# Optimization experiments

Hardware: AMD Instinct MI355X
Metric: run time of the kernel (lower is better)

The kernel has to match this reference:

```python
import jax, jax.numpy as jnp
import numpy as np
from jax import lax

KH, KW = 3, 3  # hardcoded in the original extract_patches sizes=(1,3,3,1)


def setup_inputs() -> dict:
    key = jax.random.key(0)
    k1, k2, k3 = jax.random.split(key, 3)
    B, H, W, C = 32, 56, 56, 128
    num_och = 256
    x = jax.random.normal(k1, (B, H, W, C), dtype=jnp.float32)
    w = jax.random.normal(k2, (num_och, KH * KW * C), dtype=jnp.float32) * 0.05
    b = jax.random.normal(k3, (num_och,), dtype=jnp.float32) * 0.05
    return {"x": x, "w": w, "b": b}


def reference(x, w, b):
    # Original: extract_patches (SAME, stride 1, 3x3) -> tile num_och times ->
    # elementwise multiply with w -> reduce_sum over patch axis -> + bias.
    # This is exactly a 3x3 SAME conv: patch layout is (ky, kx, cin) row-major,
    # matching tf.image.extract_patches depth ordering.
    num_och = w.shape[0]
    cin = x.shape[-1]
    # (num_och, KH*KW*C) -> (KH, KW, C, num_och) for HWIO kernel layout
    kernel = w.reshape(num_och, KH, KW, cin).transpose(1, 2, 3, 0)
    out = lax.conv_general_dilated(
        x, kernel,
        window_strides=(1, 1),
        padding="SAME",
        dimension_numbers=("NHWC", "HWIO", "NHWC"),
    )
    return out + b
```

## Files before the change

### kernel.cpp

```cpp
#include <hip/hip_runtime.h>
#include <hip/hip_bf16.h>

#define HH   56
#define WW_  56
#define CIN  128
#define OCH  256
#define NPIX (32*56*56)
#define NX   (NPIX*CIN)
#define NW   (OCH*9*CIN)
#define XB_BYTES ((size_t)NX*2)
#define WB_BYTES ((size_t)NW*2)
#define ZP_OFF   (XB_BYTES + WB_BYTES)
#define WS_NEEDED (ZP_OFF + 256)

#define NT   18
#define SLOT 65536
#define THREADS 512

typedef __attribute__((ext_vector_type(8))) short bf16x8;
typedef __attribute__((ext_vector_type(4))) float f32x4;
typedef __attribute__((address_space(1))) void v_g;
typedef __attribute__((address_space(3))) void v_l;

__device__ __forceinline__ unsigned short f2bf(float f) {
  union { float f; unsigned u; } v; v.f = f;
  unsigned r = v.u + 0x7FFF + ((v.u >> 16) & 1);
  return (unsigned short)(r >> 16);
}

__global__ __launch_bounds__(256) void convert_kern(
    const float* __restrict__ x, const float* __restrict__ w,
    char* __restrict__ ws)
{
  if (blockIdx.x == 0 && threadIdx.x < 64)
    ((float*)(ws + ZP_OFF))[threadIdx.x] = 0.f;

  unsigned short* out = (unsigned short*)ws;
  const int NT8 = (NX + NW) / 8;
  for (int i = blockIdx.x * blockDim.x + threadIdx.x; i < NT8;
       i += gridDim.x * blockDim.x) {
    const int e = i * 8;
    const float* src = (e < NX) ? (x + e) : (w + (e - NX));
    const float4 a = ((const float4*)src)[0];
    const float4 b = ((const float4*)src)[1];
    union { bf16x8 v; unsigned short u[8]; } p;
    p.u[0] = f2bf(a.x); p.u[1] = f2bf(a.y); p.u[2] = f2bf(a.z); p.u[3] = f2bf(a.w);
    p.u[4] = f2bf(b.x); p.u[5] = f2bf(b.y); p.u[6] = f2bf(b.z); p.u[7] = f2bf(b.w);
    *(bf16x8*)(out + e) = p.v;
  }
}

__global__ __launch_bounds__(THREADS, 2) void conv_gemm6(
    const char* __restrict__ ws, const float* __restrict__ bias,
    float* __restrict__ out)
{
  __shared__ char lds[2 * SLOT];

  const char* xb = ws;
  const char* wb = ws + XB_BYTES;
  const char* zp = ws + ZP_OFF;

  const int tid  = threadIdx.x;
  const int lane = tid & 63;

  const int bid = blockIdx.x;
  const int m0  = ((bid & 7) * 49 + (bid >> 3)) * 256;

  const int r0  = tid >> 3;
  const int chk = ((tid & 7) ^ (r0 & 7)) * 16;
  const char* zpc = zp + chk;

  int pixA[4], phA[4], pwA[4];
  const char* bsrc[4];
#pragma unroll
  for (int l = 0; l < 4; ++l) {
    const int r  = r0 + l * 64;
    const int p  = m0 + r;
    const int pb = p / 3136;
    const int phw = p - pb * 3136;
    phA[l] = phw / 56;
    pwA[l] = phw - phA[l] * 56;
    pixA[l] = p;
    bsrc[l] = wb + (size_t)r * 2304 + chk;
  }

  const int fr = lane & 15;
  const int fq = lane >> 4;
  const int wv = tid >> 6;
  const int wr = wv >> 2;
  const int wc = wv & 3;

  int aoffs[8], boffs[4];
#pragma unroll
  for (int mi = 0; mi < 8; ++mi) {
    const int r = wr * 128 + mi * 16 + fr;
    aoffs[mi] = r * 128 + ((fq * 16) ^ ((r & 7) << 4));
  }
#pragma unroll
  for (int nj = 0; nj < 4; ++nj) {
    const int c = wc * 64 + nj * 16 + fr;
    boffs[nj] = 32768 + c * 128 + ((fq * 16) ^ ((c & 7) << 4));
  }

  f32x4 acc[8][4];
  const f32x4 zero4 = {0.f, 0.f, 0.f, 0.f};
#pragma unroll
  for (int mi = 0; mi < 8; ++mi)
#pragma unroll
    for (int nj = 0; nj < 4; ++nj) acc[mi][nj] = zero4;

#define STAGE(tt, dst) do {                                                   \
    const int kpos_ = (tt) >> 1, kh_ = (tt) & 1;                              \
    const int ky_ = kpos_ / 3;                                                \
    const int dy_ = ky_ - 1, dx_ = kpos_ - ky_ * 3 - 1;                       \
    _Pragma("unroll")                                                         \
    for (int l = 0; l < 4; ++l) {                                             \
      const int ih_ = phA[l] + dy_, iw_ = pwA[l] + dx_;                       \
      const bool v_ = ((unsigned)ih_ < 56u) & ((unsigned)iw_ < 56u);          \
      const char* ga_ = v_ ? (xb + (size_t)(pixA[l] + dy_ * 56 + dx_) * 256   \
                                 + kh_ * 128 + chk)                           \
                           : zpc;                                             \
      __builtin_amdgcn_global_load_lds((const v_g*)ga_,                       \
          (v_l*)((dst) + l * 8192 + tid * 16), 16, 0, 0);                     \
    }                                                                         \
    _Pragma("unroll")                                                         \
    for (int l = 0; l < 4; ++l)                                               \
      __builtin_amdgcn_global_load_lds((const v_g*)(bsrc[l] + (tt) * 128),    \
          (v_l*)((dst) + 32768 + l * 8192 + tid * 16), 16, 0, 0);             \
  } while (0)

#define PHASE(src, ks, mq, LOADB) do {                                        \
    bf16x8 Aq[4];                                                             \
    _Pragma("unroll")                                                         \
    for (int i = 0; i < 4; ++i)                                               \
      Aq[i] = *(const bf16x8*)((src) + (aoffs[(mq) * 4 + i] ^ ((ks) << 6)));  \
    if (LOADB) {                                                              \
      _Pragma("unroll")                                                       \
      for (int j = 0; j < 4; ++j)                                             \
        Bq[j] = *(const bf16x8*)((src) + (boffs[j] ^ ((ks) << 6)));           \
    }                                                                         \
    __builtin_amdgcn_sched_barrier(0);                                        \
    __builtin_amdgcn_s_barrier();                                             \
    __builtin_amdgcn_sched_barrier(0);                                        \
    __builtin_amdgcn_s_setprio(1);                                            \
    _Pragma("unroll")                                                         \
    for (int i = 0; i < 4; ++i)                                               \
      _Pragma("unroll")                                                       \
      for (int j = 0; j < 4; ++j)                                             \
        acc[(mq) * 4 + i][j] = __builtin_amdgcn_mfma_f32_16x16x32_bf16(       \
            Aq[i], Bq[j], acc[(mq) * 4 + i][j], 0, 0, 0);                     \
    __builtin_amdgcn_s_setprio(0);                                            \
    __builtin_amdgcn_sched_barrier(0);                                        \
    __builtin_amdgcn_s_barrier();                                             \
  } while (0)

#define COMPUTE(src) do {                                                     \
    bf16x8 Bq[4];                                                             \
    PHASE(src, 0, 0, true);                                                   \
    PHASE(src, 0, 1, false);                                                  \
    PHASE(src, 1, 0, true);                                                   \
    PHASE(src, 1, 1, false);                                                  \
  } while (0)

  char* s0 = lds;
  char* s1 = lds + SLOT;

  STAGE(0, s0);

#pragma unroll
  for (int t = 0; t < NT - 1; ++t) {
    STAGE(t + 1, ((t + 1) & 1) ? s1 : s0);
    asm volatile("s_waitcnt vmcnt(8)" ::: "memory");
    __builtin_amdgcn_s_barrier();
    __builtin_amdgcn_sched_barrier(0);
    COMPUTE((t & 1) ? s1 : s0);
  }

  asm volatile("s_waitcnt vmcnt(0)" ::: "memory");
  __builtin_amdgcn_s_barrier();
  __builtin_amdgcn_sched_barrier(0);
  COMPUTE(((NT - 1) & 1) ? s1 : s0);

#undef STAGE
#undef PHASE
#undef COMPUTE

  float bv[4];
#pragma unroll
  for (int nj = 0; nj < 4; ++nj) bv[nj] = bias[wc * 64 + nj * 16 + fr];

#pragma unroll
  for (int mi = 0; mi < 8; ++mi) {
#pragma unroll
    for (int j = 0; j < 4; ++j) {
      const int prow = m0 + wr * 128 + mi * 16 + fq * 4 + j;
      float* orow = out + (size_t)prow * OCH + wc * 64 + fr;
#pragma unroll
      for (int nj = 0; nj < 4; ++nj)
        orow[nj * 16] = acc[mi][nj][j] + bv[nj];
    }
  }
}

__global__ __launch_bounds__(256) void conv3x3_mfma_fb(
    const float* __restrict__ x, const float* __restrict__ w,
    const float* __restrict__ bias, float* __restrict__ out)
{
  __shared__ alignas(16) unsigned char As[128 * 64];
  __shared__ alignas(16) unsigned char Bs[128 * 64];

  const int tid = threadIdx.x;
  const int m0 = (blockIdx.x >> 1) * 128;
  const int n0 = (blockIdx.x & 1) * 128;

  const int srow = tid >> 1;
  const int soff = (tid & 1) * 16;

  const int p   = m0 + srow;
  const int pb  = p / (HH * WW_);
  const int phw = p - pb * (HH * WW_);
  const int ph  = phw / WW_;
  const int pw  = phw - ph * WW_;

  const float* xrow = x + ((size_t)((pb * HH + ph) * WW_ + pw)) * CIN + soff;
  const float* wrow = w + (size_t)(n0 + srow) * (9 * CIN) + soff;

  const int sw0 = (srow * 64 + soff * 2)      ^ ((srow & 7) << 4);
  const int sw1 = (srow * 64 + soff * 2 + 16) ^ ((srow & 7) << 4);

  const int lane = tid & 63;
  const int wv = tid >> 6;
  const int wm = (wv >> 1) * 64;
  const int wn = (wv & 1) * 64;
  const int fr = lane & 15;
  const int fq = lane >> 4;

  int aoff[4], boff[4];
#pragma unroll
  for (int i = 0; i < 4; ++i) {
    const int r = wm + i * 16 + fr;
    aoff[i] = (r * 64 + fq * 16) ^ ((r & 7) << 4);
    const int c = wn + i * 16 + fr;
    boff[i] = (c * 64 + fq * 16) ^ ((c & 7) << 4);
  }

  f32x4 acc[4][4];
  const f32x4 zero4 = {0.f, 0.f, 0.f, 0.f};
#pragma unroll
  for (int i = 0; i < 4; ++i)
#pragma unroll
    for (int j = 0; j < 4; ++j) acc[i][j] = zero4;

#pragma unroll 1
  for (int kpos = 0; kpos < 9; ++kpos) {
    const int ky = kpos / 3;
    const int kx = kpos - ky * 3;
    const int ih = ph + ky - 1;
    const int iw = pw + kx - 1;
    const bool valid = ((unsigned)ih < (unsigned)HH) & ((unsigned)iw < (unsigned)WW_);
    const float* asrc = xrow + ((ky - 1) * WW_ + (kx - 1)) * CIN;
    const float* bsrc2 = wrow + kpos * CIN;

#pragma unroll 1
    for (int kc = 0; kc < 4; ++kc) {
      float4 a0, a1, a2, a3;
      if (valid) {
        const float4* s = (const float4*)(asrc + kc * 32);
        a0 = s[0]; a1 = s[1]; a2 = s[2]; a3 = s[3];
      } else {
        a0 = make_float4(0.f, 0.f, 0.f, 0.f);
        a1 = a0; a2 = a0; a3 = a0;
      }
      const float4* tql = (const float4*)(bsrc2 + kc * 32);
      const float4 b0 = tql[0], b1 = tql[1], b2 = tql[2], b3 = tql[3];

      __syncthreads();

      union { bf16x8 v; unsigned short u[8]; } pA0, pA1, pB0, pB1;
      pA0.u[0] = f2bf(a0.x); pA0.u[1] = f2bf(a0.y); pA0.u[2] = f2bf(a0.z); pA0.u[3] = f2bf(a0.w);
      pA0.u[4] = f2bf(a1.x); pA0.u[5] = f2bf(a1.y); pA0.u[6] = f2bf(a1.z); pA0.u[7] = f2bf(a1.w);
      pA1.u[0] = f2bf(a2.x); pA1.u[1] = f2bf(a2.y); pA1.u[2] = f2bf(a2.z); pA1.u[3] = f2bf(a2.w);
      pA1.u[4] = f2bf(a3.x); pA1.u[5] = f2bf(a3.y); pA1.u[6] = f2bf(a3.z); pA1.u[7] = f2bf(a3.w);
      pB0.u[0] = f2bf(b0.x); pB0.u[1] = f2bf(b0.y); pB0.u[2] = f2bf(b0.z); pB0.u[3] = f2bf(b0.w);
      pB0.u[4] = f2bf(b1.x); pB0.u[5] = f2bf(b1.y); pB0.u[6] = f2bf(b1.z); pB0.u[7] = f2bf(b1.w);
      pB1.u[0] = f2bf(b2.x); pB1.u[1] = f2bf(b2.y); pB1.u[2] = f2bf(b2.z); pB1.u[3] = f2bf(b2.w);
      pB1.u[4] = f2bf(b3.x); pB1.u[5] = f2bf(b3.y); pB1.u[6] = f2bf(b3.z); pB1.u[7] = f2bf(b3.w);

      *(bf16x8*)(As + sw0) = pA0.v;
      *(bf16x8*)(As + sw1) = pA1.v;
      *(bf16x8*)(Bs + sw0) = pB0.v;
      *(bf16x8*)(Bs + sw1) = pB1.v;

      __syncthreads();

      bf16x8 af[4], bfr[4];
#pragma unroll
      for (int i = 0; i < 4; ++i) af[i]  = *(const bf16x8*)(As + aoff[i]);
#pragma unroll
      for (int j = 0; j < 4; ++j) bfr[j] = *(const bf16x8*)(Bs + boff[j]);
#pragma unroll
      for (int i = 0; i < 4; ++i)
#pragma unroll
        for (int j = 0; j < 4; ++j)
          acc[i][j] = __builtin_amdgcn_mfma_f32_16x16x32_bf16(af[i], bfr[j], acc[i][j], 0, 0, 0);
    }
  }

  float bv[4];
#pragma unroll
  for (int j = 0; j < 4; ++j) bv[j] = bias[n0 + wn + j * 16 + fr];

#pragma unroll
  for (int mi = 0; mi < 4; ++mi) {
#pragma unroll
    for (int j = 0; j < 4; ++j) {
      const int prow = m0 + wm + mi * 16 + fq * 4 + j;
      float* orow = out + (size_t)prow * OCH + n0 + wn + fr;
#pragma unroll
      for (int ni = 0; ni < 4; ++ni)
        orow[ni * 16] = acc[mi][ni][j] + bv[ni];
    }
  }
}

extern "C" void kernel_launch(void* const* d_in, const int* in_sizes, int n_in,
                              void* d_out, int out_size, void* d_ws, size_t ws_size,
                              hipStream_t stream) {
  (void)in_sizes; (void)n_in; (void)out_size;
  const float* x = (const float*)d_in[0];
  const float* w = (const float*)d_in[1];
  const float* b = (const float*)d_in[2];
  float* out = (float*)d_out;

  if (ws_size >= WS_NEEDED) {
    convert_kern<<<dim3(2048), dim3(256), 0, stream>>>(x, w, (char*)d_ws);
    const int grid = NPIX / 256;
    conv_gemm6<<<dim3(grid), dim3(THREADS), 0, stream>>>((const char*)d_ws, b, out);
  } else {
    conv3x3_mfma_fb<<<dim3((NPIX / 128) * 2), dim3(256), 0, stream>>>(x, w, b, out);
  }
}
```

Baseline: 207.7 us.

## Software-pipeline LDS fragment loads and split global staging across MFMA phases

Restructures the main GEMM loop so the LDS register fragments for the next phase are loaded while the current phase's MFMAs run, with separate A/B buffers. The global-to-LDS staging of the next K-tile is split into two halves spread across the first two compute phases. The wait for the next tile moves to the end of the last phase, and the prologue now waits on the full first tile before starting. This aims to hide LDS read latency and spread memory issue, at the cost of more vector registers, which may pressure occupancy at 2 waves per SIMD.

```diff
diff --git a/kernel.cpp b/kernel.cpp
--- a/kernel.cpp
+++ b/kernel.cpp
@@ -50,7 +50,7 @@
   }
 }
 
-__global__ __launch_bounds__(THREADS, 2) void conv_gemm6(
+__global__ __launch_bounds__(THREADS, 2) void conv_gemm7(
     const char* __restrict__ ws, const float* __restrict__ bias,
     float* __restrict__ out)
 {
@@ -109,12 +109,12 @@
 #pragma unroll
     for (int nj = 0; nj < 4; ++nj) acc[mi][nj] = zero4;
 
-#define STAGE(tt, dst) do {                                                   \
+#define STAGE_A2(tt, dst, l0) do {                                            \
     const int kpos_ = (tt) >> 1, kh_ = (tt) & 1;                              \
     const int ky_ = kpos_ / 3;                                                \
     const int dy_ = ky_ - 1, dx_ = kpos_ - ky_ * 3 - 1;                       \
     _Pragma("unroll")                                                         \
-    for (int l = 0; l < 4; ++l) {                                             \
+    for (int l = (l0); l < (l0) + 2; ++l) {                                   \
       const int ih_ = phA[l] + dy_, iw_ = pwA[l] + dx_;                       \
       const bool v_ = ((unsigned)ih_ < 56u) & ((unsigned)iw_ < 56u);          \
       const char* ga_ = v_ ? (xb + (size_t)(pixA[l] + dy_ * 56 + dx_) * 256   \
@@ -123,67 +123,92 @@
       __builtin_amdgcn_global_load_lds((const v_g*)ga_,                       \
           (v_l*)((dst) + l * 8192 + tid * 16), 16, 0, 0);                     \
     }                                                                         \
-    _Pragma("unroll")                                                         \
-    for (int l = 0; l < 4; ++l)                                               \
+  } while (0)
+#define STAGE_B2(tt, dst, l0) do {                                            \
+    _Pragma("unroll")                                                         \
+    for (int l = (l0); l < (l0) + 2; ++l)                                     \
       __builtin_amdgcn_global_load_lds((const v_g*)(bsrc[l] + (tt) * 128),    \
           (v_l*)((dst) + 32768 + l * 8192 + tid * 16), 16, 0, 0);             \
   } while (0)
 
-#define PHASE(src, ks, mq, LOADB) do {                                        \
-    bf16x8 Aq[4];                                                             \
+#define LDA(dstbuf, src, ks, mq) do {                                         \
     _Pragma("unroll")                                                         \
     for (int i = 0; i < 4; ++i)                                               \
-      Aq[i] = *(const bf16x8*)((src) + (aoffs[(mq) * 4 + i] ^ ((ks) << 6)));  \
-    if (LOADB) {                                                              \
-      _Pragma("unroll")                                                       \
-      for (int j = 0; j < 4; ++j)                                             \
-        Bq[j] = *(const bf16x8*)((src) + (boffs[j] ^ ((ks) << 6)));           \
-    }                                                                         \
-    __builtin_amdgcn_sched_barrier(0);                                        \
-    __builtin_amdgcn_s_barrier();                                             \
-    __builtin_amdgcn_sched_barrier(0);                                        \
+      dstbuf[i] = *(const bf16x8*)((src) + (aoffs[(mq) * 4 + i] ^ ((ks) << 6)));\
+  } while (0)
+#define LDB(dstbuf, src, ks) do {                                             \
+    _Pragma("unroll")                                                         \
+    for (int j = 0; j < 4; ++j)                                               \
+      dstbuf[j] = *(const bf16x8*)((src) + (boffs[j] ^ ((ks) << 6)));         \
+  } while (0)
+
+#define MFMA16(Ab, Bb, q) do {                                                \
     __builtin_amdgcn_s_setprio(1);                                            \
     _Pragma("unroll")                                                         \
     for (int i = 0; i < 4; ++i)                                               \
       _Pragma("unroll")                                                       \
       for (int j = 0; j < 4; ++j)                                             \
-        acc[(mq) * 4 + i][j] = __builtin_amdgcn_mfma_f32_16x16x32_bf16(       \
-            Aq[i], Bq[j], acc[(mq) * 4 + i][j], 0, 0, 0);                     \
+        acc[(q) * 4 + i][j] = __builtin_amdgcn_mfma_f32_16x16x32_bf16(        \
+            Ab[i], Bb[j], acc[(q) * 4 + i][j], 0, 0, 0);                      \
     __builtin_amdgcn_s_setprio(0);                                            \
-    __builtin_amdgcn_sched_barrier(0);                                        \
-    __builtin_amdgcn_s_barrier();                                             \
-  } while (0)
-
-#define COMPUTE(src) do {                                                     \
-    bf16x8 Bq[4];                                                             \
-    PHASE(src, 0, 0, true);                                                   \
-    PHASE(src, 0, 1, false);                                                  \
-    PHASE(src, 1, 0, true);                                                   \
-    PHASE(src, 1, 1, false);                                                  \
-  } while (0)
+  } while (0)
+
+#define SBAR  __builtin_amdgcn_s_barrier()
+#define SCHED __builtin_amdgcn_sched_barrier(0)
 
   char* s0 = lds;
   char* s1 = lds + SLOT;
 
-  STAGE(0, s0);
-
-#pragma unroll
-  for (int t = 0; t < NT - 1; ++t) {
-    STAGE(t + 1, ((t + 1) & 1) ? s1 : s0);
-    asm volatile("s_waitcnt vmcnt(8)" ::: "memory");
-    __builtin_amdgcn_s_barrier();
-    __builtin_amdgcn_sched_barrier(0);
-    COMPUTE((t & 1) ? s1 : s0);
-  }
-
+  STAGE_A2(0, s0, 0); STAGE_A2(0, s0, 2);
+  STAGE_B2(0, s0, 0); STAGE_B2(0, s0, 2);
   asm volatile("s_waitcnt vmcnt(0)" ::: "memory");
-  __builtin_amdgcn_s_barrier();
-  __builtin_amdgcn_sched_barrier(0);
-  COMPUTE(((NT - 1) & 1) ? s1 : s0);
-
-#undef STAGE
-#undef PHASE
-#undef COMPUTE
+  SBAR;
+
+  bf16x8 A0[4], A1[4], A2[4], A3[4], B0[4], B1[4];
+  LDA(A0, s0, 0, 0);
+  LDB(B0, s0, 0);
+
+#pragma unroll
+  for (int t = 0; t < NT; ++t) {
+    char* src = (t & 1) ? s1 : s0;
+    char* nxt = (t & 1) ? s0 : s1;
+
+    LDA(A1, src, 0, 1);
+    if (t < NT - 1) { STAGE_A2(t + 1, nxt, 0); STAGE_B2(t + 1, nxt, 0); }
+    SCHED; SBAR; SCHED;
+    MFMA16(A0, B0, 0);
+    SCHED; SBAR;
+
+    LDA(A2, src, 1, 0);
+    LDB(B1, src, 1);
+    if (t < NT - 1) { STAGE_A2(t + 1, nxt, 2); STAGE_B2(t + 1, nxt, 2); }
+    SCHED; SBAR; SCHED;
+    MFMA16(A1, B0, 1);
+    SCHED; SBAR;
+
+    LDA(A3, src, 1, 1);
+    SCHED; SBAR; SCHED;
+    MFMA16(A2, B1, 0);
+    SCHED; SBAR;
+
+    SCHED; SBAR; SCHED;
+    MFMA16(A3, B1, 1);
+    if (t < NT - 1) asm volatile("s_waitcnt vmcnt(0)" ::: "memory");
+    SCHED; SBAR;
+
+    if (t < NT - 1) {
+      LDA(A0, nxt, 0, 0);
+      LDB(B0, nxt, 0);
+    }
+  }
+
+#undef STAGE_A2
+#undef STAGE_B2
+#undef LDA
+#undef LDB
+#undef MFMA16
+#undef SBAR
+#undef SCHED
 
   float bv[4];
 #pragma unroll
@@ -335,7 +360,7 @@
   if (ws_size >= WS_NEEDED) {
     convert_kern<<<dim3(2048), dim3(256), 0, stream>>>(x, w, (char*)d_ws);
     const int grid = NPIX / 256;
-    conv_gemm6<<<dim3(grid), dim3(THREADS), 0, stream>>>((const char*)d_ws, b, out);
+    conv_gemm7<<<dim3(grid), dim3(THREADS), 0, stream>>>((const char*)d_ws, b, out);
   } else {
     conv3x3_mfma_fb<<<dim3((NPIX / 128) * 2), dim3(256), 0, stream>>>(x, w, b, out);
   }
```

Measured after the change: 203.5 us. 2.0% less time.
